# Kernel tuning notes

Measured on AMD Instinct MI355X. Metric: run time of the kernel, lower is better.

Reference implementation:

```python
import jax, jax.numpy as jnp
import numpy as np

N_NODES = 50000
NNZ = 800000
HYPER_DIM = 128
N_LAYERS = 2
LEAKY = 0.2
LN_EPS = 1e-5


def setup_inputs() -> dict:
    key = jax.random.key(0)
    k1, k2, k3, k4 = jax.random.split(key, 4)
    return {
        "ego_embeddings": jax.random.normal(k1, (N_NODES, HYPER_DIM), dtype=jnp.float32),
        "adj_vals": jax.random.uniform(k2, (NNZ,), dtype=jnp.float32),
        "ln_gamma": jnp.ones((N_LAYERS, HYPER_DIM), dtype=jnp.float32),
        "ln_beta": jnp.zeros((N_LAYERS, HYPER_DIM), dtype=jnp.float32),
        "adj_rows": jax.random.randint(k3, (NNZ,), 0, N_NODES, dtype=jnp.int32),
        "adj_cols": jax.random.randint(k4, (NNZ,), 0, N_NODES, dtype=jnp.int32),
        "n_users": 25000,
    }


def _spmm(rows, cols, vals, x, n_out):
    # y = A @ x for sparse A in COO (rows, cols, vals): gather + segment-sum
    return jax.ops.segment_sum(vals[:, None] * x[cols], rows, num_segments=n_out)


def _layer_norm(x, gamma, beta):
    mu = jnp.mean(x, axis=-1, keepdims=True)
    var = jnp.mean(jnp.square(x - mu), axis=-1, keepdims=True)
    return (x - mu) * jax.lax.rsqrt(var + LN_EPS) * gamma + beta


def reference(ego_embeddings, adj_vals, ln_gamma, ln_beta, adj_rows, adj_cols, n_users):
    res = ego_embeddings
    embs = ego_embeddings
    for k in range(N_LAYERS):
        # adj.T @ embs  (rows of A^T are cols of A)
        ht = _spmm(adj_cols, adj_rows, adj_vals, embs, N_NODES)
        # adj @ (adj.T @ embs)
        h = _spmm(adj_rows, adj_cols, adj_vals, ht, N_NODES)
        if k != N_LAYERS - 1:
            h = jnp.where(h >= 0, h, LEAKY * h)  # LeakyReLU
        embs = _layer_norm(h, ln_gamma[k], ln_beta[k]) + res
    user_emb = embs[:n_users]
    item_emb = embs[n_users:]
    return (user_emb, item_emb)
```

## Files before the change

### kernel.cpp

```cpp
#include <hip/hip_runtime.h>
#include <hip/hip_bf16.h>

#define HD 128
#define PB 512
#define CAP 20480
#define LEAKY 0.2f
#define LN_EPS 1e-5f

__device__ __forceinline__ unsigned short bfr(float f) {
    unsigned int b = __float_as_uint(f);
    return (unsigned short)((b + 0x7fffu + ((b >> 16) & 1u)) >> 16);
}
__device__ __forceinline__ float blo(unsigned int u) { return __uint_as_float(u << 16); }
__device__ __forceinline__ float bhi(unsigned int u) { return __uint_as_float(u & 0xffff0000u); }

__global__ __launch_bounds__(256) void scatter_direct(
    const int* __restrict__ rows, const int* __restrict__ cols,
    const float* __restrict__ vals,
    const float* __restrict__ ego, unsigned short* __restrict__ ego_bf,
    int* __restrict__ gcur,
    unsigned* __restrict__ pay_r, unsigned short* __restrict__ bin_r,
    unsigned* __restrict__ pay_c, unsigned short* __restrict__ bin_c,
    int nnz, int n4) {
    __shared__ int cR[64], cC[64], wbR[64], wbC[64];
    if (threadIdx.x < 64) { cR[threadIdx.x] = 0; cC[threadIdx.x] = 0; }
    __syncthreads();
    int chunk = (nnz + PB - 1) / PB;
    int beg = blockIdx.x * chunk;
    int end = min(beg + chunk, nnz);
    for (int i = beg + threadIdx.x; i < end; i += 256) {
        atomicAdd(&cR[rows[i] >> 10], 1);
        atomicAdd(&cC[cols[i] >> 10], 1);
    }
    for (int i = blockIdx.x * 256 + threadIdx.x; i < n4; i += 256 * PB) {
        float4 f = ((const float4*)ego)[i];
        ushort4 u;
        u.x = bfr(f.x); u.y = bfr(f.y); u.z = bfr(f.z); u.w = bfr(f.w);
        ((ushort4*)ego_bf)[i] = u;
    }
    __syncthreads();
    if (threadIdx.x < 64) {
        int t = threadIdx.x;
        wbR[t] = cR[t] ? atomicAdd(&gcur[t], cR[t]) : 0;
        wbC[t] = cC[t] ? atomicAdd(&gcur[64 + t], cC[t]) : 0;
        cR[t] = 0; cC[t] = 0;
    }
    __syncthreads();
    for (int i = beg + threadIdx.x; i < end; i += 256) {
        int ro = rows[i], co = cols[i];
        unsigned vb = (unsigned)bfr(vals[i]) << 16;
        int bk = ro >> 10;
        int rk = atomicAdd(&cR[bk], 1);
        int idx = bk * CAP + wbR[bk] + rk;
        pay_r[idx] = vb | (unsigned)co;
        bin_r[idx] = (unsigned short)(ro & 1023);
        bk = co >> 10;
        rk = atomicAdd(&cC[bk], 1);
        idx = bk * CAP + wbC[bk] + rk;
        pay_c[idx] = vb | (unsigned)ro;
        bin_c[idx] = (unsigned short)(co & 1023);
    }
}

__global__ __launch_bounds__(1024) void bucket_build(
    const unsigned* __restrict__ pay_r, const unsigned short* __restrict__ bin_r,
    const unsigned* __restrict__ pay_c, const unsigned short* __restrict__ bin_c,
    const int* __restrict__ gcur,
    unsigned* __restrict__ ent_r, unsigned* __restrict__ ent_c,
    int* __restrict__ rp_r, int* __restrict__ rp_c,
    int n, int nnz, int nbk) {
    __shared__ int cnt[1024];
    __shared__ int wsum[16], woff[16];
    __shared__ int s_base;
    int bkt = blockIdx.x, dir = blockIdx.y;
    const unsigned* pay = dir ? pay_c : pay_r;
    const unsigned short* bin = dir ? bin_c : bin_r;
    unsigned* ent = dir ? ent_c : ent_r;
    int* rp = dir ? rp_c : rp_r;
    if (threadIdx.x < 64) {
        int v = (threadIdx.x < bkt) ? gcur[dir * 64 + threadIdx.x] : 0;
        #pragma unroll
        for (int off = 32; off; off >>= 1) v += __shfl_xor(v, off);
        if (threadIdx.x == 0) s_base = v;
    }
    cnt[threadIdx.x] = 0;
    __syncthreads();
    int base = s_base;
    int total = gcur[dir * 64 + bkt];
    int lo = bkt << 10;
    int nb = min(1024, n - lo);
    const unsigned short* bb = bin + (size_t)bkt * CAP;
    const unsigned* pb = pay + (size_t)bkt * CAP;
    for (int i = threadIdx.x; i < total; i += 1024)
        atomicAdd(&cnt[bb[i]], 1);
    __syncthreads();
    int lane = threadIdx.x & 63, wid = threadIdx.x >> 6;
    int v = cnt[threadIdx.x];
    int incl = v;
    #pragma unroll
    for (int off = 1; off < 64; off <<= 1) {
        int t = __shfl_up(incl, off);
        if (lane >= off) incl += t;
    }
    if (lane == 63) wsum[wid] = incl;
    __syncthreads();
    if (threadIdx.x == 0) {
        int run = 0;
        #pragma unroll
        for (int w = 0; w < 16; ++w) { woff[w] = run; run += wsum[w]; }
    }
    __syncthreads();
    int excl = woff[wid] + incl - v;
    if (threadIdx.x < nb) rp[lo + threadIdx.x] = base + excl;
    if (bkt == nbk - 1 && threadIdx.x == 0) rp[n] = nnz;
    cnt[threadIdx.x] = excl;
    __syncthreads();
    for (int i = threadIdx.x; i < total; i += 1024) {
        int pos = atomicAdd(&cnt[bb[i]], 1);
        ent[base + pos] = pb[i];
    }
}

__global__ __launch_bounds__(256) void spmm_bf(
    const unsigned short* __restrict__ x, const int* __restrict__ rp,
    const unsigned* __restrict__ ent,
    const unsigned short* __restrict__ res, const float* __restrict__ gamma,
    const float* __restrict__ beta,
    unsigned short* __restrict__ out_bf, float* __restrict__ out_f32,
    int n, int post) {
    int wid = threadIdx.x >> 6, lane = threadIdx.x & 63;
    int row = blockIdx.x * 4 + wid;
    if (row >= n) return;
    int quarter = lane >> 4, q = lane & 15;
    int beg = rp[row], end = rp[row + 1];
    float acc[8];
    #pragma unroll
    for (int k = 0; k < 8; ++k) acc[k] = 0.f;

    int i = beg + quarter;
    for (; i + 12 < end; i += 16) {
        unsigned e0 = ent[i], e1 = ent[i + 4], e2 = ent[i + 8], e3 = ent[i + 12];
        uint4 u0 = ((const uint4*)(x + (size_t)(e0 & 0xffffu) * HD))[q];
        uint4 u1 = ((const uint4*)(x + (size_t)(e1 & 0xffffu) * HD))[q];
        uint4 u2 = ((const uint4*)(x + (size_t)(e2 & 0xffffu) * HD))[q];
        uint4 u3 = ((const uint4*)(x + (size_t)(e3 & 0xffffu) * HD))[q];
        float v0 = bhi(e0), v1 = bhi(e1), v2 = bhi(e2), v3 = bhi(e3);
        acc[0] += v0 * blo(u0.x) + v1 * blo(u1.x);
        acc[1] += v0 * bhi(u0.x) + v1 * bhi(u1.x);
        acc[2] += v0 * blo(u0.y) + v1 * blo(u1.y);
        acc[3] += v0 * bhi(u0.y) + v1 * bhi(u1.y);
        acc[4] += v0 * blo(u0.z) + v1 * blo(u1.z);
        acc[5] += v0 * bhi(u0.z) + v1 * bhi(u1.z);
        acc[6] += v0 * blo(u0.w) + v1 * blo(u1.w);
        acc[7] += v0 * bhi(u0.w) + v1 * bhi(u1.w);
        acc[0] += v2 * blo(u2.x) + v3 * blo(u3.x);
        acc[1] += v2 * bhi(u2.x) + v3 * bhi(u3.x);
        acc[2] += v2 * blo(u2.y) + v3 * blo(u3.y);
        acc[3] += v2 * bhi(u2.y) + v3 * bhi(u3.y);
        acc[4] += v2 * blo(u2.z) + v3 * blo(u3.z);
        acc[5] += v2 * bhi(u2.z) + v3 * bhi(u3.z);
        acc[6] += v2 * blo(u2.w) + v3 * blo(u3.w);
        acc[7] += v2 * bhi(u2.w) + v3 * bhi(u3.w);
    }
    for (; i < end; i += 4) {
        unsigned e0 = ent[i];
        uint4 u0 = ((const uint4*)(x + (size_t)(e0 & 0xffffu) * HD))[q];
        float v0 = bhi(e0);
        acc[0] += v0 * blo(u0.x);
        acc[1] += v0 * bhi(u0.x);
        acc[2] += v0 * blo(u0.y);
        acc[3] += v0 * bhi(u0.y);
        acc[4] += v0 * blo(u0.z);
        acc[5] += v0 * bhi(u0.z);
        acc[6] += v0 * blo(u0.w);
        acc[7] += v0 * bhi(u0.w);
    }
    #pragma unroll
    for (int k = 0; k < 8; ++k) {
        acc[k] += __shfl_xor(acc[k], 16);
        acc[k] += __shfl_xor(acc[k], 32);
    }
    if (quarter != 0) return;

    if (post == 0) {
        uint4 s;
        s.x = (unsigned)bfr(acc[0]) | ((unsigned)bfr(acc[1]) << 16);
        s.y = (unsigned)bfr(acc[2]) | ((unsigned)bfr(acc[3]) << 16);
        s.z = (unsigned)bfr(acc[4]) | ((unsigned)bfr(acc[5]) << 16);
        s.w = (unsigned)bfr(acc[6]) | ((unsigned)bfr(acc[7]) << 16);
        ((uint4*)(out_bf + (size_t)row * HD))[q] = s;
        return;
    }
    if (post == 1) {
        #pragma unroll
        for (int k = 0; k < 8; ++k) acc[k] = acc[k] >= 0.f ? acc[k] : LEAKY * acc[k];
    }
    float t = 0.f;
    #pragma unroll
    for (int k = 0; k < 8; ++k) t += acc[k];
    #pragma unroll
    for (int off = 1; off < 16; off <<= 1) t += __shfl_xor(t, off);
    float mu = t * (1.f / HD);
    float d[8], vs = 0.f;
    #pragma unroll
    for (int k = 0; k < 8; ++k) { d[k] = acc[k] - mu; vs += d[k] * d[k]; }
    #pragma unroll
    for (int off = 1; off < 16; off <<= 1) vs += __shfl_xor(vs, off);
    float inv = rsqrtf(vs * (1.f / HD) + LN_EPS);

    float4 g0 = ((const float4*)gamma)[2 * q], g1 = ((const float4*)gamma)[2 * q + 1];
    float4 b0 = ((const float4*)beta)[2 * q],  b1 = ((const float4*)beta)[2 * q + 1];
    uint4 ru = ((const uint4*)(res + (size_t)row * HD))[q];
    float o[8];
    o[0] = d[0] * inv * g0.x + b0.x + blo(ru.x);
    o[1] = d[1] * inv * g0.y + b0.y + bhi(ru.x);
    o[2] = d[2] * inv * g0.z + b0.z + blo(ru.y);
    o[3] = d[3] * inv * g0.w + b0.w + bhi(ru.y);
    o[4] = d[4] * inv * g1.x + b1.x + blo(ru.z);
    o[5] = d[5] * inv * g1.y + b1.y + bhi(ru.z);
    o[6] = d[6] * inv * g1.z + b1.z + blo(ru.w);
    o[7] = d[7] * inv * g1.w + b1.w + bhi(ru.w);
    if (post == 1) {
        uint4 s;
        s.x = (unsigned)bfr(o[0]) | ((unsigned)bfr(o[1]) << 16);
        s.y = (unsigned)bfr(o[2]) | ((unsigned)bfr(o[3]) << 16);
        s.z = (unsigned)bfr(o[4]) | ((unsigned)bfr(o[5]) << 16);
        s.w = (unsigned)bfr(o[6]) | ((unsigned)bfr(o[7]) << 16);
        ((uint4*)(out_bf + (size_t)row * HD))[q] = s;
    } else {
        float4 s0 = {o[0], o[1], o[2], o[3]};
        float4 s1 = {o[4], o[5], o[6], o[7]};
        ((float4*)(out_f32 + (size_t)row * HD))[2 * q] = s0;
        ((float4*)(out_f32 + (size_t)row * HD))[2 * q + 1] = s1;
    }
}

extern "C" void kernel_launch(void* const* d_in, const int* in_sizes, int n_in,
                              void* d_out, int out_size, void* d_ws, size_t ws_size,
                              hipStream_t stream) {
    const float* ego   = (const float*)d_in[0];
    const float* vals  = (const float*)d_in[1];
    const float* gamma = (const float*)d_in[2];
    const float* beta  = (const float*)d_in[3];
    const int*   rows  = (const int*)d_in[4];
    const int*   cols  = (const int*)d_in[5];

    const int N   = in_sizes[0] / HD;
    const int NNZ = in_sizes[1];
    const int NBK = (N + 1023) >> 10;

    float* out = (float*)d_out;
    char* w = (char*)d_ws;
    unsigned short* ego_bf = (unsigned short*)w; w += (size_t)N * HD * 2;
    unsigned short* bufA   = (unsigned short*)w; w += (size_t)N * HD * 2;
    unsigned short* bufB   = (unsigned short*)w; w += (size_t)N * HD * 2;
    int*  rp_r = (int*)w;  w += (size_t)(N + 8) * 4;
    int*  rp_c = (int*)w;  w += (size_t)(N + 8) * 4;
    unsigned* ent_r = (unsigned*)w; w += (size_t)NNZ * 4;
    unsigned* ent_c = (unsigned*)w; w += (size_t)NNZ * 4;
    unsigned* pay_r = (unsigned*)w; w += (size_t)64 * CAP * 4;
    unsigned* pay_c = (unsigned*)w; w += (size_t)64 * CAP * 4;
    unsigned short* bin_r = (unsigned short*)w; w += (size_t)64 * CAP * 2;
    unsigned short* bin_c = (unsigned short*)w; w += (size_t)64 * CAP * 2;
    int* gcur = (int*)w; w += 128 * 4;

    hipMemsetAsync(gcur, 0, 128 * 4, stream);
    scatter_direct<<<PB, 256, 0, stream>>>(rows, cols, vals, ego, ego_bf, gcur,
                                           pay_r, bin_r, pay_c, bin_c,
                                           NNZ, N * HD / 4);
    bucket_build<<<dim3(NBK, 2), 1024, 0, stream>>>(pay_r, bin_r, pay_c, bin_c,
                                                    gcur, ent_r, ent_c,
                                                    rp_r, rp_c, N, NNZ, NBK);

    const int sblocks = (N + 3) / 4;

    spmm_bf<<<sblocks, 256, 0, stream>>>(ego_bf, rp_c, ent_c,
                                         nullptr, nullptr, nullptr, bufA, nullptr, N, 0);
    spmm_bf<<<sblocks, 256, 0, stream>>>(bufA, rp_r, ent_r,
                                         ego_bf, gamma, beta, bufB, nullptr, N, 1);
    spmm_bf<<<sblocks, 256, 0, stream>>>(bufB, rp_c, ent_c,
                                         nullptr, nullptr, nullptr, bufA, nullptr, N, 0);
    spmm_bf<<<sblocks, 256, 0, stream>>>(bufA, rp_r, ent_r,
                                         ego_bf, gamma + HD, beta + HD, nullptr, out, N, 2);
}
```

Baseline: 272.9 us.

## Split each CSR row into four source-range segments to localize gathers

```diff
diff --git a/kernel.cpp b/kernel.cpp
--- a/kernel.cpp
+++ b/kernel.cpp
@@ -4,6 +4,7 @@
 #define HD 128
 #define PB 512
 #define CAP 20480
+#define SEG 4
 #define LEAKY 0.2f
 #define LN_EPS 1e-5f
 
@@ -67,23 +68,24 @@
     const unsigned* __restrict__ pay_c, const unsigned short* __restrict__ bin_c,
     const int* __restrict__ gcur,
     unsigned* __restrict__ ent_r, unsigned* __restrict__ ent_c,
-    int* __restrict__ rp_r, int* __restrict__ rp_c,
-    int n, int nnz, int nbk) {
-    __shared__ int cnt[1024];
+    int* __restrict__ rp4_r, int* __restrict__ rp4_c,
+    int n, int nnz, int nbk, float segscale) {
+    __shared__ int cnt[1024 * SEG];
     __shared__ int wsum[16], woff[16];
     __shared__ int s_base;
     int bkt = blockIdx.x, dir = blockIdx.y;
     const unsigned* pay = dir ? pay_c : pay_r;
     const unsigned short* bin = dir ? bin_c : bin_r;
     unsigned* ent = dir ? ent_c : ent_r;
-    int* rp = dir ? rp_c : rp_r;
+    int* rp4 = dir ? rp4_c : rp4_r;
     if (threadIdx.x < 64) {
         int v = (threadIdx.x < bkt) ? gcur[dir * 64 + threadIdx.x] : 0;
         #pragma unroll
         for (int off = 32; off; off >>= 1) v += __shfl_xor(v, off);
         if (threadIdx.x == 0) s_base = v;
     }
-    cnt[threadIdx.x] = 0;
+    #pragma unroll
+    for (int s = 0; s < SEG; ++s) cnt[threadIdx.x + s * 1024] = 0;
     __syncthreads();
     int base = s_base;
     int total = gcur[dir * 64 + bkt];
@@ -91,12 +93,17 @@
     int nb = min(1024, n - lo);
     const unsigned short* bb = bin + (size_t)bkt * CAP;
     const unsigned* pb = pay + (size_t)bkt * CAP;
-    for (int i = threadIdx.x; i < total; i += 1024)
-        atomicAdd(&cnt[bb[i]], 1);
+    for (int i = threadIdx.x; i < total; i += 1024) {
+        int src = (int)(pb[i] & 0xffffu);
+        int sg = min(SEG - 1, (int)((float)src * segscale));
+        atomicAdd(&cnt[((int)bb[i] << 2) | sg], 1);
+    }
     __syncthreads();
     int lane = threadIdx.x & 63, wid = threadIdx.x >> 6;
-    int v = cnt[threadIdx.x];
-    int incl = v;
+    int t4 = threadIdx.x << 2;
+    int v0 = cnt[t4], v1 = cnt[t4 + 1], v2 = cnt[t4 + 2], v3 = cnt[t4 + 3];
+    int s = v0 + v1 + v2 + v3;
+    int incl = s;
     #pragma unroll
     for (int off = 1; off < 64; off <<= 1) {
         int t = __shfl_up(incl, off);
@@ -110,19 +117,31 @@
         for (int w = 0; w < 16; ++w) { woff[w] = run; run += wsum[w]; }
     }
     __syncthreads();
-    int excl = woff[wid] + incl - v;
-    if (threadIdx.x < nb) rp[lo + threadIdx.x] = base + excl;
-    if (bkt == nbk - 1 && threadIdx.x == 0) rp[n] = nnz;
-    cnt[threadIdx.x] = excl;
+    int excl = woff[wid] + incl - s;
+    cnt[t4] = excl;
+    cnt[t4 + 1] = excl + v0;
+    cnt[t4 + 2] = excl + v0 + v1;
+    cnt[t4 + 3] = excl + v0 + v1 + v2;
+    __syncthreads();
+    if (threadIdx.x < nb) {
+        int b4 = threadIdx.x << 2;
+        int4 r = make_int4(base + cnt[b4], base + cnt[b4 + 1],
+                           base + cnt[b4 + 2], base + cnt[b4 + 3]);
+        ((int4*)(rp4 + ((size_t)(lo + threadIdx.x) << 2)))[0] = r;
+    }
+    if (bkt == nbk - 1 && threadIdx.x == 0) rp4[(size_t)n << 2] = nnz;
     __syncthreads();
     for (int i = threadIdx.x; i < total; i += 1024) {
-        int pos = atomicAdd(&cnt[bb[i]], 1);
-        ent[base + pos] = pb[i];
+        unsigned p = pb[i];
+        int src = (int)(p & 0xffffu);
+        int sg = min(SEG - 1, (int)((float)src * segscale));
+        int pos = atomicAdd(&cnt[((int)bb[i] << 2) | sg], 1);
+        ent[base + pos] = p;
     }
 }
 
 __global__ __launch_bounds__(256) void spmm_bf(
-    const unsigned short* __restrict__ x, const int* __restrict__ rp,
+    const unsigned short* __restrict__ x, const int* __restrict__ rp4,
     const unsigned* __restrict__ ent,
     const unsigned short* __restrict__ res, const float* __restrict__ gamma,
     const float* __restrict__ beta,
@@ -132,48 +151,45 @@
     int row = blockIdx.x * 4 + wid;
     if (row >= n) return;
     int quarter = lane >> 4, q = lane & 15;
-    int beg = rp[row], end = rp[row + 1];
+    int r4 = row << 2;
+    int4 st = ((const int4*)(rp4 + r4))[0];
+    int nxt = rp4[r4 + 4];
+    int bgs[5] = {st.x, st.y, st.z, st.w, nxt};
     float acc[8];
     #pragma unroll
     for (int k = 0; k < 8; ++k) acc[k] = 0.f;
 
-    int i = beg + quarter;
-    for (; i + 12 < end; i += 16) {
-        unsigned e0 = ent[i], e1 = ent[i + 4], e2 = ent[i + 8], e3 = ent[i + 12];
-        uint4 u0 = ((const uint4*)(x + (size_t)(e0 & 0xffffu) * HD))[q];
-        uint4 u1 = ((const uint4*)(x + (size_t)(e1 & 0xffffu) * HD))[q];
-        uint4 u2 = ((const uint4*)(x + (size_t)(e2 & 0xffffu) * HD))[q];
-        uint4 u3 = ((const uint4*)(x + (size_t)(e3 & 0xffffu) * HD))[q];
-        float v0 = bhi(e0), v1 = bhi(e1), v2 = bhi(e2), v3 = bhi(e3);
-        acc[0] += v0 * blo(u0.x) + v1 * blo(u1.x);
-        acc[1] += v0 * bhi(u0.x) + v1 * bhi(u1.x);
-        acc[2] += v0 * blo(u0.y) + v1 * blo(u1.y);
-        acc[3] += v0 * bhi(u0.y) + v1 * bhi(u1.y);
-        acc[4] += v0 * blo(u0.z) + v1 * blo(u1.z);
-        acc[5] += v0 * bhi(u0.z) + v1 * bhi(u1.z);
-        acc[6] += v0 * blo(u0.w) + v1 * blo(u1.w);
-        acc[7] += v0 * bhi(u0.w) + v1 * bhi(u1.w);
-        acc[0] += v2 * blo(u2.x) + v3 * blo(u3.x);
-        acc[1] += v2 * bhi(u2.x) + v3 * bhi(u3.x);
-        acc[2] += v2 * blo(u2.y) + v3 * blo(u3.y);
-        acc[3] += v2 * bhi(u2.y) + v3 * bhi(u3.y);
-        acc[4] += v2 * blo(u2.z) + v3 * blo(u3.z);
-        acc[5] += v2 * bhi(u2.z) + v3 * bhi(u3.z);
-        acc[6] += v2 * blo(u2.w) + v3 * blo(u3.w);
-        acc[7] += v2 * bhi(u2.w) + v3 * bhi(u3.w);
-    }
-    for (; i < end; i += 4) {
-        unsigned e0 = ent[i];
-        uint4 u0 = ((const uint4*)(x + (size_t)(e0 & 0xffffu) * HD))[q];
-        float v0 = bhi(e0);
-        acc[0] += v0 * blo(u0.x);
-        acc[1] += v0 * bhi(u0.x);
-        acc[2] += v0 * blo(u0.y);
-        acc[3] += v0 * bhi(u0.y);
-        acc[4] += v0 * blo(u0.z);
-        acc[5] += v0 * bhi(u0.z);
-        acc[6] += v0 * blo(u0.w);
-        acc[7] += v0 * bhi(u0.w);
+    #pragma unroll
+    for (int p = 0; p < SEG; ++p) {
+        int i = bgs[p] + quarter;
+        int ep = bgs[p + 1];
+        for (; i + 4 < ep; i += 8) {
+            unsigned e0 = ent[i], e1 = ent[i + 4];
+            uint4 u0 = ((const uint4*)(x + (size_t)(e0 & 0xffffu) * HD))[q];
+            uint4 u1 = ((const uint4*)(x + (size_t)(e1 & 0xffffu) * HD))[q];
+            float v0 = bhi(e0), v1 = bhi(e1);
+            acc[0] += v0 * blo(u0.x) + v1 * blo(u1.x);
+            acc[1] += v0 * bhi(u0.x) + v1 * bhi(u1.x);
+            acc[2] += v0 * blo(u0.y) + v1 * blo(u1.y);
+            acc[3] += v0 * bhi(u0.y) + v1 * bhi(u1.y);
+            acc[4] += v0 * blo(u0.z) + v1 * blo(u1.z);
+            acc[5] += v0 * bhi(u0.z) + v1 * bhi(u1.z);
+            acc[6] += v0 * blo(u0.w) + v1 * blo(u1.w);
+            acc[7] += v0 * bhi(u0.w) + v1 * bhi(u1.w);
+        }
+        for (; i < ep; i += 4) {
+            unsigned e0 = ent[i];
+            uint4 u0 = ((const uint4*)(x + (size_t)(e0 & 0xffffu) * HD))[q];
+            float v0 = bhi(e0);
+            acc[0] += v0 * blo(u0.x);
+            acc[1] += v0 * bhi(u0.x);
+            acc[2] += v0 * blo(u0.y);
+            acc[3] += v0 * bhi(u0.y);
+            acc[4] += v0 * blo(u0.z);
+            acc[5] += v0 * bhi(u0.z);
+            acc[6] += v0 * blo(u0.w);
+            acc[7] += v0 * bhi(u0.w);
+        }
     }
     #pragma unroll
     for (int k = 0; k < 8; ++k) {
@@ -248,14 +264,15 @@
     const int N   = in_sizes[0] / HD;
     const int NNZ = in_sizes[1];
     const int NBK = (N + 1023) >> 10;
+    const float segscale = (float)SEG / (float)N;
 
     float* out = (float*)d_out;
     char* w = (char*)d_ws;
     unsigned short* ego_bf = (unsigned short*)w; w += (size_t)N * HD * 2;
     unsigned short* bufA   = (unsigned short*)w; w += (size_t)N * HD * 2;
     unsigned short* bufB   = (unsigned short*)w; w += (size_t)N * HD * 2;
-    int*  rp_r = (int*)w;  w += (size_t)(N + 8) * 4;
-    int*  rp_c = (int*)w;  w += (size_t)(N + 8) * 4;
+    int* rp4_r = (int*)w;  w += (size_t)(N * 4 + 8) * 4;
+    int* rp4_c = (int*)w;  w += (size_t)(N * 4 + 8) * 4;
     unsigned* ent_r = (unsigned*)w; w += (size_t)NNZ * 4;
     unsigned* ent_c = (unsigned*)w; w += (size_t)NNZ * 4;
     unsigned* pay_r = (unsigned*)w; w += (size_t)64 * CAP * 4;
@@ -270,16 +287,17 @@
                                            NNZ, N * HD / 4);
     bucket_build<<<dim3(NBK, 2), 1024, 0, stream>>>(pay_r, bin_r, pay_c, bin_c,
                                                     gcur, ent_r, ent_c,
-                                                    rp_r, rp_c, N, NNZ, NBK);
+                                                    rp4_r, rp4_c, N, NNZ, NBK,
+                                                    segscale);
 
     const int sblocks = (N + 3) / 4;
 
-    spmm_bf<<<sblocks, 256, 0, stream>>>(ego_bf, rp_c, ent_c,
+    spmm_bf<<<sblocks, 256, 0, stream>>>(ego_bf, rp4_c, ent_c,
                                          nullptr, nullptr, nullptr, bufA, nullptr, N, 0);
-    spmm_bf<<<sblocks, 256, 0, stream>>>(bufA, rp_r, ent_r,
+    spmm_bf<<<sblocks, 256, 0, stream>>>(bufA, rp4_r, ent_r,
                                          ego_bf, gamma, beta, bufB, nullptr, N, 1);
-    spmm_bf<<<sblocks, 256, 0, stream>>>(bufB, rp_c, ent_c,
+    spmm_bf<<<sblocks, 256, 0, stream>>>(bufB, rp4_c, ent_c,
                                          nullptr, nullptr, nullptr, bufA, nullptr, N, 0);
-    spmm_bf<<<sblocks, 256, 0, stream>>>(bufA, rp_r, ent_r,
+    spmm_bf<<<sblocks, 256, 0, stream>>>(bufA, rp4_r, ent_r,
                                          ego_bf, gamma + HD, beta + HD, nullptr, out, N, 2);
 }
```

After: 297.7 us. 9.1% more time.
